# Kernel optimization log

Measured on AMD Instinct MI355X. Metric: run time of the kernel, lower is better.

The kernel has to match this reference:

```python
import jax, jax.numpy as jnp
import numpy as np

KERNEL_NUM = 21
SIGMA = 0.1
EXACT_SIGMA = 0.001

def _kernel_params():
    mus, sigmas = [], []
    for i in range(KERNEL_NUM):
        mu = 1.0 / (KERNEL_NUM - 1) + 2.0 * i / (KERNEL_NUM - 1) - 1.0
        sigma = SIGMA
        if mu > 1.0:
            sigma = EXACT_SIGMA
            mu = 1.0
        mus.append(mu)
        sigmas.append(sigma)
    return np.asarray(mus, np.float32), np.asarray(sigmas, np.float32)

MU, SIG = _kernel_params()  # [K], [K]

def setup_inputs() -> dict:
    key = jax.random.key(0)
    k = jax.random.split(key, 8)
    V, D, B, L, R = 50000, 128, 512, 30, 200
    emb = jax.random.normal(k[0], (V, D), dtype=jnp.float32)
    W = jax.random.normal(k[1], (1, KERNEL_NUM), dtype=jnp.float32) * 0.1
    b = jax.random.normal(k[2], (1,), dtype=jnp.float32) * 0.1
    query1 = jax.random.randint(k[3], (B, L), 0, V, dtype=jnp.int32)
    doc1 = jax.random.randint(k[4], (B, R), 0, V, dtype=jnp.int32)
    query2 = jax.random.randint(k[5], (B, L), 0, V, dtype=jnp.int32)
    doc2 = jax.random.randint(k[6], (B, R), 0, V, dtype=jnp.int32)
    return {"emb": emb, "W": W, "b": b, "query1": query1, "doc1": doc1,
            "query2": query2, "doc2": doc2}

def _l2norm(x):
    # F.normalize(p=2, dim=-1): x / max(||x||, eps)
    n = jnp.sqrt(jnp.sum(x * x, axis=-1, keepdims=True))
    return x / jnp.maximum(n, 1e-12)

def _predict(emb, W, b, q, d):
    eq = _l2norm(emb[q])              # [B,L,D]
    ed = _l2norm(emb[d])              # [B,R,D]
    M = jnp.einsum('bld,brd->blr', eq, ed)  # matching matrix [B,L,R]
    # multi-Gaussian kernel bank: [B,L,R,K]
    Kmat = jnp.exp(-0.5 * (M[..., None] - MU) ** 2 / (SIG ** 2))
    km = jnp.sum(jnp.log1p(jnp.sum(Kmat, axis=2)), axis=1)  # [B,K]
    return km @ W.T + b               # [B,1]

def reference(emb, W, b, query1, doc1, query2, doc2):
    logits1 = _predict(emb, W, b, query1, doc1)
    logits2 = _predict(emb, W, b, query2, doc2)
    return jax.nn.sigmoid(logits1 - logits2)
```

## Files before the change

kernel.cpp:

```cpp
#include <hip/hip_runtime.h>
#include <hip/hip_fp16.h>
#include <math.h>

#define V   50000
#define DIM 128
#define BB  512
#define LQ  30
#define RD  200
#define KN  21

typedef __attribute__((ext_vector_type(8))) _Float16 f16x8;
typedef __attribute__((ext_vector_type(4))) float f32x4;
typedef __attribute__((ext_vector_type(2))) float f32x2;

#if __has_builtin(__builtin_amdgcn_exp2f)
#define EXP2F(x) __builtin_amdgcn_exp2f(x)
#else
#define EXP2F(x) __expf((x) * 0.69314718f)
#endif

#define ALPHA 72.1347520f
#define E10   22026.4657948f

static __device__ __forceinline__ f16x8 as_hfrag(int4 v) {
    return __builtin_bit_cast(f16x8, v);
}
static __device__ __forceinline__ unsigned pk2h(float a, float b) {
    return __builtin_bit_cast(unsigned, __builtin_amdgcn_cvt_pkrtz(a, b));
}
static __device__ __forceinline__ unsigned hscale(unsigned u, __half2 s) {
    return __builtin_bit_cast(unsigned, __hmul2(__builtin_bit_cast(__half2, u), s));
}

static __device__ __forceinline__ void gather_row_f16(const float* __restrict__ rowp,
                                                      int g, int4* f) {
    float ss = 0.0f;
#pragma unroll
    for (int ks = 0; ks < 4; ++ks) {
        const float4* p = reinterpret_cast<const float4*>(rowp + ks * 32 + g * 8);
        float4 a = p[0], b = p[1];
        ss = fmaf(a.x, a.x, fmaf(a.y, a.y, fmaf(a.z, a.z, fmaf(a.w, a.w, ss))));
        ss = fmaf(b.x, b.x, fmaf(b.y, b.y, fmaf(b.z, b.z, fmaf(b.w, b.w, ss))));
        f[ks].x = (int)pk2h(a.x, a.y);
        f[ks].y = (int)pk2h(a.z, a.w);
        f[ks].z = (int)pk2h(b.x, b.y);
        f[ks].w = (int)pk2h(b.z, b.w);
    }
    ss += __shfl_xor(ss, 16);
    ss += __shfl_xor(ss, 32);
    const float inv = rsqrtf(fmaxf(ss, 1e-24f));
    const __half2 h2 = __float2half2_rn(inv);
#pragma unroll
    for (int ks = 0; ks < 4; ++ks) {
        f[ks].x = (int)hscale((unsigned)f[ks].x, h2);
        f[ks].y = (int)hscale((unsigned)f[ks].y, h2);
        f[ks].z = (int)hscale((unsigned)f[ks].z, h2);
        f[ks].w = (int)hscale((unsigned)f[ks].w, h2);
    }
}

static __device__ __forceinline__ void bank4_pk(f32x4 pv, int4 dt, int qt,
                                                f32x2* ks2, float& cnt) {
    const float mv[4] = {pv[0], pv[1], pv[2], pv[3]};
    const int   dv[4] = {dt.x, dt.y, dt.z, dt.w};
    f32x2 t[4], u[4];
#pragma unroll
    for (int i = 0; i < 4; ++i) {
        float m  = mv[i];
        float dA = m + 0.5f, dB = m - 0.5f;
        float tA = EXP2F(-ALPHA * dA * (dA + 0.9f));
        float tB = EXP2F(-ALPHA * dB * (dB + 0.9f));
        float uB = EXP2F(14.4269504f * dB);
        float uA = uB * E10;
        t[i] = f32x2{tA, tB};
        u[i] = f32x2{uA, uB};
        cnt += (dv[i] == qt) ? 1.0f : 0.0f;
    }
#pragma unroll
    for (int k = 0; k < 10; ++k) {
        ks2[k] += (t[0] + t[1]) + (t[2] + t[3]);
        t[0] *= u[0]; t[1] *= u[1]; t[2] *= u[2]; t[3] *= u[3];
    }
}

__global__ __launch_bounds__(256, 4) void knrm_main(
    const float* __restrict__ emb, const float* __restrict__ W,
    const int* __restrict__ q1, const int* __restrict__ d1,
    const int* __restrict__ q2, const int* __restrict__ d2,
    float* __restrict__ logits)
{
    __shared__ int sQtok[32];
    __shared__ __align__(16) int sDtok[256];
    __shared__ int4 sQ[32][16];
    __shared__ float kred[4][32][KN];

    const int pb = blockIdx.x;
    const int pair = pb >> 9, b = pb & 511;
    const int* qind = (pair ? q2 : q1) + b * LQ;
    const int* dind = (pair ? d2 : d1) + b * RD;

    const int tid = threadIdx.x;
    const int lane = tid & 63, w = tid >> 6;
    const int r = lane & 15, g = lane >> 4;

    if (tid < 32) sQtok[tid] = (tid < LQ) ? qind[tid] : -2;
    sDtok[tid] = dind[tid < RD ? tid : RD - 1];

    {
        const int row = tid >> 3, seg = tid & 7;
        const int qi = qind[row < LQ ? row : LQ - 1];
        const float4* p = reinterpret_cast<const float4*>(emb + (size_t)qi * DIM + seg * 16);
        float4 v0 = p[0], v1 = p[1], v2 = p[2], v3 = p[3];
        float s0 = 0.f, s1 = 0.f, s2 = 0.f, s3 = 0.f;
        s0 = fmaf(v0.x, v0.x, fmaf(v0.y, v0.y, s0)); s1 = fmaf(v0.z, v0.z, fmaf(v0.w, v0.w, s1));
        s2 = fmaf(v1.x, v1.x, fmaf(v1.y, v1.y, s2)); s3 = fmaf(v1.z, v1.z, fmaf(v1.w, v1.w, s3));
        s0 = fmaf(v2.x, v2.x, fmaf(v2.y, v2.y, s0)); s1 = fmaf(v2.z, v2.z, fmaf(v2.w, v2.w, s1));
        s2 = fmaf(v3.x, v3.x, fmaf(v3.y, v3.y, s2)); s3 = fmaf(v3.z, v3.z, fmaf(v3.w, v3.w, s3));
        float ss = (s0 + s1) + (s2 + s3);
        ss += __shfl_xor(ss, 1);
        ss += __shfl_xor(ss, 2);
        ss += __shfl_xor(ss, 4);
        const float inv = rsqrtf(fmaxf(ss, 1e-24f));
        int4 t0, t1;
        t0.x = (int)pk2h(v0.x * inv, v0.y * inv);
        t0.y = (int)pk2h(v0.z * inv, v0.w * inv);
        t0.z = (int)pk2h(v1.x * inv, v1.y * inv);
        t0.w = (int)pk2h(v1.z * inv, v1.w * inv);
        t1.x = (int)pk2h(v2.x * inv, v2.y * inv);
        t1.y = (int)pk2h(v2.z * inv, v2.w * inv);
        t1.z = (int)pk2h(v3.x * inv, v3.y * inv);
        t1.w = (int)pk2h(v3.z * inv, v3.w * inv);
        const int rw = row & 15;
        sQ[row][(2 * seg) ^ rw]     = t0;
        sQ[row][(2 * seg + 1) ^ rw] = t1;
    }
    __syncthreads();

    int4 qa[4], qb[4];
#pragma unroll
    for (int ks = 0; ks < 4; ++ks) {
        qa[ks] = sQ[r][(ks * 4 + g) ^ r];
        qb[ks] = sQ[16 + r][(ks * 4 + g) ^ r];
    }
    const int qt0 = sQtok[r], qt1 = sQtok[16 + r];
    const int4* sDtok4 = (const int4*)sDtok;

    f32x2 ks0[10], ks1[10];
#pragma unroll
    for (int k = 0; k < 10; ++k) { ks0[k] = f32x2{0.f, 0.f}; ks1[k] = f32x2{0.f, 0.f}; }
    float cnt0 = 0.0f, cnt1 = 0.0f;

    auto strip = [&](int sbase) {
        const int di = sDtok[sbase + r];
        int4 df[4];
        gather_row_f16(emb + (size_t)di * DIM, g, df);
        f32x4 acc0 = {0.f, 0.f, 0.f, 0.f}, acc1 = {0.f, 0.f, 0.f, 0.f};
#pragma unroll
        for (int ks = 0; ks < 4; ++ks) {
            f16x8 fd = as_hfrag(df[ks]);
            acc0 = __builtin_amdgcn_mfma_f32_16x16x32_f16(fd, as_hfrag(qa[ks]), acc0, 0, 0, 0);
            acc1 = __builtin_amdgcn_mfma_f32_16x16x32_f16(fd, as_hfrag(qb[ks]), acc1, 0, 0, 0);
        }
        if (sbase + g * 4 < RD) {
            const int4 dt = sDtok4[(sbase >> 2) + g];
            bank4_pk(acc0, dt, qt0, ks0, cnt0);
            bank4_pk(acc1, dt, qt1, ks1, cnt1);
        }
    };

    if (w < 3) {
#pragma unroll 2
        for (int s = 0; s < 4; ++s) strip(w * 64 + s * 16);
    } else {
        strip(192);
    }

#pragma unroll
    for (int k = 0; k < 10; ++k) {
        float a0 = ks0[k].x, b0 = ks0[k].y, a1 = ks1[k].x, b1 = ks1[k].y;
        a0 += __shfl_xor(a0, 16); a0 += __shfl_xor(a0, 32);
        b0 += __shfl_xor(b0, 16); b0 += __shfl_xor(b0, 32);
        a1 += __shfl_xor(a1, 16); a1 += __shfl_xor(a1, 32);
        b1 += __shfl_xor(b1, 16); b1 += __shfl_xor(b1, 32);
        ks0[k] = f32x2{a0, b0};
        ks1[k] = f32x2{a1, b1};
    }
    cnt0 += __shfl_xor(cnt0, 16); cnt0 += __shfl_xor(cnt0, 32);
    cnt1 += __shfl_xor(cnt1, 16); cnt1 += __shfl_xor(cnt1, 32);

    if (lane < 16) {
        float* k0 = &kred[w][r][0];
        float* k1 = &kred[w][16 + r][0];
#pragma unroll
        for (int k = 0; k < 10; ++k) {
            k0[k] = ks0[k].x;  k0[10 + k] = ks0[k].y;
            k1[k] = ks1[k].x;  k1[10 + k] = ks1[k].y;
        }
        k0[20] = cnt0;
        k1[20] = cnt1;
    }
    __syncthreads();

    if (tid < 64) {
        float part = 0.0f;
        if (tid < LQ) {
#pragma unroll
            for (int k = 0; k < KN; ++k) {
                float s = kred[0][tid][k] + kred[1][tid][k]
                        + kred[2][tid][k] + kred[3][tid][k];
                float sc = 1.0f;
                if (k < 20) {
                    float j = (float)((k < 10) ? k : k - 10) - 4.5f;
                    sc = EXP2F(-0.721347520f * j * j);
                }
                part += W[k] * log1pf(sc * s);
            }
        }
        part += __shfl_xor(part, 1);
        part += __shfl_xor(part, 2);
        part += __shfl_xor(part, 4);
        part += __shfl_xor(part, 8);
        part += __shfl_xor(part, 16);
        part += __shfl_xor(part, 32);
        if (tid == 0) logits[pair * BB + b] = part;
    }
}

__global__ void knrm_final(const float* __restrict__ logits, float* __restrict__ out) {
    int i = blockIdx.x * blockDim.x + threadIdx.x;
    if (i < BB) {
        float x = logits[i] - logits[BB + i];
        out[i] = 1.0f / (1.0f + expf(-x));
    }
}

extern "C" void kernel_launch(void* const* d_in, const int* in_sizes, int n_in,
                              void* d_out, int out_size, void* d_ws, size_t ws_size,
                              hipStream_t stream) {
    const float* emb = (const float*)d_in[0];
    const float* W   = (const float*)d_in[1];
    const int* q1    = (const int*)d_in[3];
    const int* dd1   = (const int*)d_in[4];
    const int* q2    = (const int*)d_in[5];
    const int* dd2   = (const int*)d_in[6];

    float* logits = (float*)d_ws;

    knrm_main<<<1024, 256, 0, stream>>>(emb, W, q1, dd1, q2, dd2, logits);
    knrm_final<<<2, 256, 0, stream>>>(logits, (float*)d_out);
}
```

Before: 33.75 us.

## Fuse both query-doc pairs into one 512-thread block and drop final kernel

Each block now handles one batch row with both pairs: eight wavefronts, four per pair. The sigmoid of the logit difference is computed in-block through shared memory, which removes the second kernel launch and the workspace round trip. It also raises the priority of the MFMA section with s_setprio. The cost is larger blocks with doubled shared memory and an extra barrier, which may limit occupancy and scheduling flexibility.

```diff
diff --git a/kernel.cpp b/kernel.cpp
--- a/kernel.cpp
+++ b/kernel.cpp
@@ -83,34 +83,40 @@
     }
 }
 
-__global__ __launch_bounds__(256, 4) void knrm_main(
+__global__ __launch_bounds__(512, 4) void knrm_main(
     const float* __restrict__ emb, const float* __restrict__ W,
     const int* __restrict__ q1, const int* __restrict__ d1,
     const int* __restrict__ q2, const int* __restrict__ d2,
-    float* __restrict__ logits)
+    float* __restrict__ out)
 {
-    __shared__ int sQtok[32];
-    __shared__ __align__(16) int sDtok[256];
-    __shared__ int4 sQ[32][16];
-    __shared__ float kred[4][32][KN];
-
-    const int pb = blockIdx.x;
-    const int pair = pb >> 9, b = pb & 511;
-    const int* qind = (pair ? q2 : q1) + b * LQ;
-    const int* dind = (pair ? d2 : d1) + b * RD;
-
+    __shared__ int sQtok[2][32];
+    __shared__ __align__(16) int sDtok[2][256];
+    __shared__ int4 sQ[2][32][16];
+    __shared__ float kred[2][4][32][KN];
+    __shared__ float lgbuf[2];
+
+    const int b = blockIdx.x;
     const int tid = threadIdx.x;
     const int lane = tid & 63, w = tid >> 6;
+    const int p = w >> 2, wl = w & 3;
     const int r = lane & 15, g = lane >> 4;
 
-    if (tid < 32) sQtok[tid] = (tid < LQ) ? qind[tid] : -2;
-    sDtok[tid] = dind[tid < RD ? tid : RD - 1];
+    const int* qind = (p ? q2 : q1) + b * LQ;
+    const int* dind = (p ? d2 : d1) + b * RD;
+
+    {
+        const int th = tid & 255;
+        if (th < 32) sQtok[p][th] = (th < LQ) ? qind[th] : -2;
+        sDtok[p][th] = dind[th < RD ? th : RD - 1];
+    }
 
     {
         const int row = tid >> 3, seg = tid & 7;
-        const int qi = qind[row < LQ ? row : LQ - 1];
-        const float4* p = reinterpret_cast<const float4*>(emb + (size_t)qi * DIM + seg * 16);
-        float4 v0 = p[0], v1 = p[1], v2 = p[2], v3 = p[3];
+        const int qp = row >> 5, prow = row & 31;
+        const int* qip = (qp ? q2 : q1) + b * LQ;
+        const int qi = qip[prow < LQ ? prow : LQ - 1];
+        const float4* pt = reinterpret_cast<const float4*>(emb + (size_t)qi * DIM + seg * 16);
+        float4 v0 = pt[0], v1 = pt[1], v2 = pt[2], v3 = pt[3];
         float s0 = 0.f, s1 = 0.f, s2 = 0.f, s3 = 0.f;
         s0 = fmaf(v0.x, v0.x, fmaf(v0.y, v0.y, s0)); s1 = fmaf(v0.z, v0.z, fmaf(v0.w, v0.w, s1));
         s2 = fmaf(v1.x, v1.x, fmaf(v1.y, v1.y, s2)); s3 = fmaf(v1.z, v1.z, fmaf(v1.w, v1.w, s3));
@@ -130,20 +136,20 @@
         t1.y = (int)pk2h(v2.z * inv, v2.w * inv);
         t1.z = (int)pk2h(v3.x * inv, v3.y * inv);
         t1.w = (int)pk2h(v3.z * inv, v3.w * inv);
-        const int rw = row & 15;
-        sQ[row][(2 * seg) ^ rw]     = t0;
-        sQ[row][(2 * seg + 1) ^ rw] = t1;
+        const int rw = prow & 15;
+        sQ[qp][prow][(2 * seg) ^ rw]     = t0;
+        sQ[qp][prow][(2 * seg + 1) ^ rw] = t1;
     }
     __syncthreads();
 
     int4 qa[4], qb[4];
 #pragma unroll
     for (int ks = 0; ks < 4; ++ks) {
-        qa[ks] = sQ[r][(ks * 4 + g) ^ r];
-        qb[ks] = sQ[16 + r][(ks * 4 + g) ^ r];
-    }
-    const int qt0 = sQtok[r], qt1 = sQtok[16 + r];
-    const int4* sDtok4 = (const int4*)sDtok;
+        qa[ks] = sQ[p][r][(ks * 4 + g) ^ r];
+        qb[ks] = sQ[p][16 + r][(ks * 4 + g) ^ r];
+    }
+    const int qt0 = sQtok[p][r], qt1 = sQtok[p][16 + r];
+    const int4* sDtok4 = (const int4*)sDtok[p];
 
     f32x2 ks0[10], ks1[10];
 #pragma unroll
@@ -151,16 +157,18 @@
     float cnt0 = 0.0f, cnt1 = 0.0f;
 
     auto strip = [&](int sbase) {
-        const int di = sDtok[sbase + r];
+        const int di = sDtok[p][sbase + r];
         int4 df[4];
         gather_row_f16(emb + (size_t)di * DIM, g, df);
         f32x4 acc0 = {0.f, 0.f, 0.f, 0.f}, acc1 = {0.f, 0.f, 0.f, 0.f};
+        __builtin_amdgcn_s_setprio(1);
 #pragma unroll
         for (int ks = 0; ks < 4; ++ks) {
             f16x8 fd = as_hfrag(df[ks]);
             acc0 = __builtin_amdgcn_mfma_f32_16x16x32_f16(fd, as_hfrag(qa[ks]), acc0, 0, 0, 0);
             acc1 = __builtin_amdgcn_mfma_f32_16x16x32_f16(fd, as_hfrag(qb[ks]), acc1, 0, 0, 0);
         }
+        __builtin_amdgcn_s_setprio(0);
         if (sbase + g * 4 < RD) {
             const int4 dt = sDtok4[(sbase >> 2) + g];
             bank4_pk(acc0, dt, qt0, ks0, cnt0);
@@ -168,9 +176,9 @@
         }
     };
 
-    if (w < 3) {
+    if (wl < 3) {
 #pragma unroll 2
-        for (int s = 0; s < 4; ++s) strip(w * 64 + s * 16);
+        for (int s = 0; s < 4; ++s) strip(wl * 64 + s * 16);
     } else {
         strip(192);
     }
@@ -189,8 +197,8 @@
     cnt1 += __shfl_xor(cnt1, 16); cnt1 += __shfl_xor(cnt1, 32);
 
     if (lane < 16) {
-        float* k0 = &kred[w][r][0];
-        float* k1 = &kred[w][16 + r][0];
+        float* k0 = &kred[p][wl][r][0];
+        float* k1 = &kred[p][wl][16 + r][0];
 #pragma unroll
         for (int k = 0; k < 10; ++k) {
             k0[k] = ks0[k].x;  k0[10 + k] = ks0[k].y;
@@ -201,13 +209,13 @@
     }
     __syncthreads();
 
-    if (tid < 64) {
+    if (wl == 0) {
         float part = 0.0f;
-        if (tid < LQ) {
+        if (lane < LQ) {
 #pragma unroll
             for (int k = 0; k < KN; ++k) {
-                float s = kred[0][tid][k] + kred[1][tid][k]
-                        + kred[2][tid][k] + kred[3][tid][k];
+                float s = kred[p][0][lane][k] + kred[p][1][lane][k]
+                        + kred[p][2][lane][k] + kred[p][3][lane][k];
                 float sc = 1.0f;
                 if (k < 20) {
                     float j = (float)((k < 10) ? k : k - 10) - 4.5f;
@@ -222,15 +230,13 @@
         part += __shfl_xor(part, 8);
         part += __shfl_xor(part, 16);
         part += __shfl_xor(part, 32);
-        if (tid == 0) logits[pair * BB + b] = part;
-    }
-}
-
-__global__ void knrm_final(const float* __restrict__ logits, float* __restrict__ out) {
-    int i = blockIdx.x * blockDim.x + threadIdx.x;
-    if (i < BB) {
-        float x = logits[i] - logits[BB + i];
-        out[i] = 1.0f / (1.0f + expf(-x));
+        if (lane == 0) lgbuf[p] = part;
+    }
+    __syncthreads();
+
+    if (tid == 0) {
+        float x = lgbuf[0] - lgbuf[1];
+        out[b] = 1.0f / (1.0f + expf(-x));
     }
 }
 
@@ -244,8 +250,5 @@
     const int* q2    = (const int*)d_in[5];
     const int* dd2   = (const int*)d_in[6];
 
-    float* logits = (float*)d_ws;
-
-    knrm_main<<<1024, 256, 0, stream>>>(emb, W, q1, dd1, q2, dd2, logits);
-    knrm_final<<<2, 256, 0, stream>>>(logits, (float*)d_out);
-}
+    knrm_main<<<BB, 512, 0, stream>>>(emb, W, q1, dd1, q2, dd2, (float*)d_out);
+}
```

Result: slower. 34.60 us (+2.5%).
